# Performance work log

Measured on AMD Instinct MI355X. Metric: run time of the kernel, lower is better.

Reference implementation:

```python
import jax, jax.numpy as jnp
import numpy as np

I, H, L, O = 11, 33, 3, 18

def lstm_layer(x_tbi, W_ih, W_hh, b_ih, b_hh):
    # x_tbi: [T, B, in]; W_ih: [4H, in]; W_hh: [4H, H]
    T, B = x_tbi.shape[0], x_tbi.shape[1]
    # precompute input contribution for all timesteps (one big GEMM)
    xg = jnp.einsum('tbi,gi->tbg', x_tbi, W_ih) + b_ih + b_hh  # [T, B, 4H]
    h0 = jnp.zeros((B, H), x_tbi.dtype)
    c0 = jnp.zeros((B, H), x_tbi.dtype)

    def step(carry, xg_t):
        h, c = carry
        gates = xg_t + h @ W_hh.T                      # [B, 4H]
        i, f, g, o = jnp.split(gates, 4, axis=-1)      # PyTorch gate order i,f,g,o
        i = jax.nn.sigmoid(i)
        f = jax.nn.sigmoid(f)
        g = jnp.tanh(g)
        o = jax.nn.sigmoid(o)
        c = f * c + i * g
        h = o * jnp.tanh(c)
        return (h, c), h

    (hT, cT), ys = jax.lax.scan(step, (h0, c0), xg)
    return ys, hT, cT  # ys: [T, B, H]


def setup_inputs() -> dict:
    key = jax.random.key(0)
    ks = jax.random.split(key, 20)
    B, T = 512, 2048
    s = 1.0 / np.sqrt(H)
    d = {'x': jax.random.normal(ks[0], (B, T, I), jnp.float32)}
    in_sizes = [I, H, H]
    for l in range(L):
        d[f'W_ih{l}'] = jax.random.uniform(ks[1 + 4 * l], (4 * H, in_sizes[l]), jnp.float32, -s, s)
        d[f'W_hh{l}'] = jax.random.uniform(ks[2 + 4 * l], (4 * H, H), jnp.float32, -s, s)
        d[f'b_ih{l}'] = jax.random.uniform(ks[3 + 4 * l], (4 * H,), jnp.float32, -s, s)
        d[f'b_hh{l}'] = jax.random.uniform(ks[4 + 4 * l], (4 * H,), jnp.float32, -s, s)
    d['W1'] = jax.random.normal(ks[13], (4 * O, H), jnp.float32) * 0.05
    d['b1'] = jnp.zeros((4 * O,), jnp.float32)
    d['W2'] = jax.random.normal(ks[14], (O, 4 * O), jnp.float32) * 0.05
    d['b2'] = jnp.zeros((O,), jnp.float32)
    return d


def reference(x, W_ih0, W_hh0, b_ih0, b_hh0, W_ih1, W_hh1, b_ih1, b_hh1,
              W_ih2, W_hh2, b_ih2, b_hh2, W1, b1, W2, b2):
    # x: [B, T, I] (batch_first) -> time-major for scan
    xt = jnp.transpose(x, (1, 0, 2))  # [T, B, I]
    params = [(W_ih0, W_hh0, b_ih0, b_hh0),
              (W_ih1, W_hh1, b_ih1, b_hh1),
              (W_ih2, W_hh2, b_ih2, b_hh2)]
    hiddens = []
    cur = xt
    for (Wi, Wh, bi, bh) in params:
        cur, hT, _ = lstm_layer(cur, Wi, Wh, bi, bh)
        hiddens.append(hT)
    hidden = jnp.stack(hiddens, axis=0)  # [L, B, H] (final hidden state per layer)
    # MLP head (dropout inactive at inference); torch nn.GELU default = exact erf
    h1 = jax.nn.gelu(hidden @ W1.T + b1, approximate=False)
    out = h1 @ W2.T + b2  # [L, B, O]
    return out, hidden
```

## Files before the change

kernel.cpp:

```cpp
#include <hip/hip_runtime.h>
#include <math.h>

#define TT 2048
#define BB 512
#define II 11
#define HH 33
#define NL 3
#define OO 18
#define HSLOT 48

typedef _Float16 h2 __attribute__((ext_vector_type(2)));
typedef _Float16 h8 __attribute__((ext_vector_type(8)));

__device__ __forceinline__ float sigm_f(float x) {
    float e = __expf(-x);
    return __builtin_amdgcn_rcpf(1.0f + e);
}
__device__ __forceinline__ float tanh_f(float x) {
    float e = __expf(2.0f * x);
    return 1.0f - 2.0f * __builtin_amdgcn_rcpf(e + 1.0f);
}

__device__ __forceinline__ h8 gldh8(const float* p, int k0, int rem) {
    h8 v;
    #pragma unroll
    for (int i = 0; i < 8; ++i) v[i] = (_Float16)((k0 + i < rem) ? p[k0 + i] : 0.0f);
    return v;
}
__device__ __forceinline__ h2 gldh2(const float* p, int k0, int rem) {
    h2 v;
    v.x = (_Float16)((k0 + 0 < rem) ? p[k0 + 0] : 0.0f);
    v.y = (_Float16)((k0 + 1 < rem) ? p[k0 + 1] : 0.0f);
    return v;
}

#define D8(a, v, w) do { \
    a = __builtin_amdgcn_fdot2((v).s01, (w).s01, a, false); \
    a = __builtin_amdgcn_fdot2((v).s23, (w).s23, a, false); \
    a = __builtin_amdgcn_fdot2((v).s45, (w).s45, a, false); \
    a = __builtin_amdgcn_fdot2((v).s67, (w).s67, a, false); } while (0)
#define D1(a, v, w) a = __builtin_amdgcn_fdot2((v), (w), a, false)

__global__ __launch_bounds__(128, 1) void lstm_pipeline_kernel(
    const float* __restrict__ x,
    const float* __restrict__ Wih0, const float* __restrict__ Whh0,
    const float* __restrict__ bih0, const float* __restrict__ bhh0,
    const float* __restrict__ Wih1, const float* __restrict__ Whh1,
    const float* __restrict__ bih1, const float* __restrict__ bhh1,
    const float* __restrict__ Wih2, const float* __restrict__ Whh2,
    const float* __restrict__ bih2, const float* __restrict__ bhh2,
    const float* __restrict__ W1, const float* __restrict__ b1,
    const float* __restrict__ W2, const float* __restrict__ b2,
    float* __restrict__ hidden_out,
    float* __restrict__ outp)
{
    __shared__ __align__(16) _Float16 buf[2][NL + 1][HSLOT];
    __shared__ float hfin[NL][HH + 1];
    __shared__ float h1s[NL][4 * OO];

    const int tid = threadIdx.x;
    const int bg  = blockIdx.x;

    for (int i = tid; i < 2 * (NL + 1) * HSLOT; i += 128)
        ((_Float16*)buf)[i] = (_Float16)0.0f;

    const bool comp = (tid < 99);
    const int  u    = tid;
    const int  l    = (u < 33) ? 0 : (u < 66) ? 1 : 2;
    const int  j    = u - 33 * l;

    const int  pi   = tid - 99;
    const bool pref = (pi >= 0) && (pi < II);
    const float* xrow = x + (size_t)bg * TT * II + (pref ? pi : 0);

    h8 z8 = {0,0,0,0,0,0,0,0};
    h2 z2 = {(_Float16)0.0f, (_Float16)0.0f};
    h8 x00=z8,x01=z8,x02=z8,x03=z8; h2 x0t=z2;
    h8 x10=z8,x11=z8,x12=z8,x13=z8; h2 x1t=z2;
    h8 x20=z8,x21=z8,x22=z8,x23=z8; h2 x2t=z2;
    h8 x30=z8,x31=z8,x32=z8,x33=z8; h2 x3t=z2;
    h8 h00=z8,h01=z8,h02=z8,h03=z8; h2 h0t=z2;
    h8 h10=z8,h11=z8,h12=z8,h13=z8; h2 h1t=z2;
    h8 h20=z8,h21=z8,h22=z8,h23=z8; h2 h2t=z2;
    h8 h30=z8,h31=z8,h32=z8,h33=z8; h2 h3t=z2;
    float b0 = 0.0f, b1v = 0.0f, b2v = 0.0f, b3v = 0.0f;

    if (comp) {
        const float* bip = (l == 0) ? bih0 : (l == 1) ? bih1 : bih2;
        const float* bhp = (l == 0) ? bhh0 : (l == 1) ? bhh1 : bhh2;
        b0  = bip[0 * HH + j] + bhp[0 * HH + j];
        b1v = bip[1 * HH + j] + bhp[1 * HH + j];
        b2v = bip[2 * HH + j] + bhp[2 * HH + j];
        b3v = bip[3 * HH + j] + bhp[3 * HH + j];

        const float* Wi = (l == 0) ? Wih0 : (l == 1) ? Wih1 : Wih2;
        const float* Wh = (l == 0) ? Whh0 : (l == 1) ? Whh1 : Whh2;
        const int kin = (l == 0) ? II : HH;
        const float* r0 = Wi + (0 * HH + j) * kin;
        const float* r1 = Wi + (1 * HH + j) * kin;
        const float* r2 = Wi + (2 * HH + j) * kin;
        const float* r3 = Wi + (3 * HH + j) * kin;
        x00=gldh8(r0,0,kin); x01=gldh8(r0,8,kin); x02=gldh8(r0,16,kin); x03=gldh8(r0,24,kin); x0t=gldh2(r0,32,kin);
        x10=gldh8(r1,0,kin); x11=gldh8(r1,8,kin); x12=gldh8(r1,16,kin); x13=gldh8(r1,24,kin); x1t=gldh2(r1,32,kin);
        x20=gldh8(r2,0,kin); x21=gldh8(r2,8,kin); x22=gldh8(r2,16,kin); x23=gldh8(r2,24,kin); x2t=gldh2(r2,32,kin);
        x30=gldh8(r3,0,kin); x31=gldh8(r3,8,kin); x32=gldh8(r3,16,kin); x33=gldh8(r3,24,kin); x3t=gldh2(r3,32,kin);
        const float* s0 = Wh + (0 * HH + j) * HH;
        const float* s1 = Wh + (1 * HH + j) * HH;
        const float* s2 = Wh + (2 * HH + j) * HH;
        const float* s3 = Wh + (3 * HH + j) * HH;
        h00=gldh8(s0,0,HH); h01=gldh8(s0,8,HH); h02=gldh8(s0,16,HH); h03=gldh8(s0,24,HH); h0t=gldh2(s0,32,HH);
        h10=gldh8(s1,0,HH); h11=gldh8(s1,8,HH); h12=gldh8(s1,16,HH); h13=gldh8(s1,24,HH); h1t=gldh2(s1,32,HH);
        h20=gldh8(s2,0,HH); h21=gldh8(s2,8,HH); h22=gldh8(s2,16,HH); h23=gldh8(s2,24,HH); h2t=gldh2(s2,32,HH);
        h30=gldh8(s3,0,HH); h31=gldh8(s3,8,HH); h32=gldh8(s3,16,HH); h33=gldh8(s3,24,HH); h3t=gldh2(s3,32,HH);
    }

    __syncthreads();
    float v_next = 0.0f, v_next2 = 0.0f;
    if (pref) {
        buf[0][0][pi] = (_Float16)xrow[0];
        v_next  = xrow[II];
        v_next2 = xrow[2 * II];
    }
    __syncthreads();

    float c = 0.0f;

    const _Float16* rin[2]  = { &buf[0][l][0],     &buf[1][l][0] };
    const _Float16* rown[2] = { &buf[0][l + 1][0], &buf[1][l + 1][0] };
    _Float16*       wrp[2]  = { &buf[0][l + 1][j], &buf[1][l + 1][j] };
    _Float16*       pxp[2]  = { &buf[0][0][pi],    &buf[1][0][pi] };

    auto step = [&](int s, int rp, bool check, bool out, bool xload, bool xstore)
        __attribute__((always_inline)) {
        const int wp = rp ^ 1;
        if (pref) {
            if (xstore) *pxp[wp] = (_Float16)v_next;
            v_next = v_next2;
            if (xload) v_next2 = xrow[(size_t)(s + 3) * II];
        }
        const bool active = check ? (comp && (s >= l) && (s - l < TT)) : comp;
        if (active) {
            const h8* VI = (const h8*)rin[rp];
            const h8 vi0 = VI[0], vi1 = VI[1], vi2 = VI[2], vi3 = VI[3];
            const h2 vit = *(const h2*)(rin[rp] + 32);
            const h8* VO = (const h8*)rown[rp];
            const h8 vo0 = VO[0], vo1 = VO[1], vo2 = VO[2], vo3 = VO[3];
            const h2 vot = *(const h2*)(rown[rp] + 32);

            float a0 = b0, a1 = b1v;
            D8(a1, vi0, x10); D8(a0, vi0, x00);
            D8(a1, vi1, x11); D8(a0, vi1, x01);
            D8(a1, vi2, x12); D8(a0, vi2, x02);
            D8(a1, vi3, x13); D8(a0, vi3, x03);
            D1(a1, vit, x1t); D1(a0, vit, x0t);
            D8(a1, vo0, h10); D8(a0, vo0, h00);
            D8(a1, vo1, h11); D8(a0, vo1, h01);
            D8(a1, vo2, h12); D8(a0, vo2, h02);
            D8(a1, vo3, h13); D8(a0, vo3, h03);
            D1(a1, vot, h1t); D1(a0, vot, h0t);
            const float fg = sigm_f(a1);
            const float ig = sigm_f(a0);

            float a2 = b2v, a3 = b3v;
            D8(a2, vi0, x20); D8(a3, vi0, x30);
            D8(a2, vi1, x21); D8(a3, vi1, x31);
            D8(a2, vi2, x22); D8(a3, vi2, x32);
            D8(a2, vi3, x23); D8(a3, vi3, x33);
            D1(a2, vit, x2t); D1(a3, vit, x3t);
            D8(a2, vo0, h20); D8(a3, vo0, h30);
            D8(a2, vo1, h21); D8(a3, vo1, h31);
            D8(a2, vo2, h22); D8(a3, vo2, h32);
            D8(a2, vo3, h23); D8(a3, vo3, h33);
            D1(a2, vot, h2t); D1(a3, vot, h3t);

            const float gg = tanh_f(a2);
            const float og = sigm_f(a3);
            c = __builtin_fmaf(fg, c, ig * gg);
            const float hnew = og * tanh_f(c);

            *wrp[wp] = (_Float16)hnew;
            if (out && (s - l == TT - 1)) {
                hidden_out[((size_t)l * BB + bg) * HH + j] = hnew;
                hfin[l][j] = hnew;
            }
        }
        __syncthreads();
    };

    step(0, 0, true, false, true, true);
    step(1, 1, true, false, true, true);
    for (int s = 2; s < TT - 4; s += 2) {
        step(s,     0, false, false, true, true);
        step(s + 1, 1, false, false, true, true);
    }
    step(TT - 4, 0, false, false, true,  true);
    step(TT - 3, 1, false, false, false, true);
    step(TT - 2, 0, false, false, false, true);
    step(TT - 1, 1, false, true,  false, false);
    step(TT,     0, true,  true,  false, false);
    step(TT + 1, 1, true,  true,  false, false);

    if (tid < 4 * OO) {
        #pragma unroll
        for (int ml = 0; ml < NL; ++ml) {
            float a = b1[tid];
            #pragma unroll
            for (int k = 0; k < HH; ++k) a += hfin[ml][k] * W1[tid * HH + k];
            h1s[ml][tid] = 0.5f * a * (1.0f + erff(a * 0.70710678118654752f));
        }
    }
    __syncthreads();
    if (tid < NL * OO) {
        const int ol = tid / OO, o = tid % OO;
        float a = b2[o];
        #pragma unroll
        for (int m = 0; m < 4 * OO; ++m) a += h1s[ol][m] * W2[o * (4 * OO) + m];
        outp[((size_t)ol * BB + bg) * OO + o] = a;
    }
}

extern "C" void kernel_launch(void* const* d_in, const int* in_sizes, int n_in,
                              void* d_out, int out_size, void* d_ws, size_t ws_size,
                              hipStream_t stream) {
    const float* x    = (const float*)d_in[0];
    const float* Wih0 = (const float*)d_in[1];
    const float* Whh0 = (const float*)d_in[2];
    const float* bih0 = (const float*)d_in[3];
    const float* bhh0 = (const float*)d_in[4];
    const float* Wih1 = (const float*)d_in[5];
    const float* Whh1 = (const float*)d_in[6];
    const float* bih1 = (const float*)d_in[7];
    const float* bhh1 = (const float*)d_in[8];
    const float* Wih2 = (const float*)d_in[9];
    const float* Whh2 = (const float*)d_in[10];
    const float* bih2 = (const float*)d_in[11];
    const float* bhh2 = (const float*)d_in[12];
    const float* W1   = (const float*)d_in[13];
    const float* b1   = (const float*)d_in[14];
    const float* W2   = (const float*)d_in[15];
    const float* b2   = (const float*)d_in[16];

    float* out    = (float*)d_out;
    float* hidden = out + NL * BB * OO;

    lstm_pipeline_kernel<<<BB, 128, 0, stream>>>(
        x, Wih0, Whh0, bih0, bhh0, Wih1, Whh1, bih1, bhh1,
        Wih2, Whh2, bih2, bhh2, W1, b1, W2, b2, hidden, out);
}
```

Before: 1.053 ms.

## Split each LSTM hidden unit across two lanes with DPP reduction

Each hidden unit is now computed by a lane pair, each lane covering half of the K dimension, and the partial gate sums are combined with a DPP quad-perm swap. The transcendental work is also split: one lane evaluates the i/g pair through a parameterised sigmoid/tanh formula and the other evaluates f/o, and the results are exchanged via DPP. Block size doubles to 256 threads with launch bounds (256,2). The aim is to shorten the serial per-timestep critical path, at the cost of extra cross-lane ops, more waves hitting each barrier, and higher register pressure per block.

```diff
diff --git a/kernel.cpp b/kernel.cpp
--- a/kernel.cpp
+++ b/kernel.cpp
@@ -21,6 +21,11 @@
     return 1.0f - 2.0f * __builtin_amdgcn_rcpf(e + 1.0f);
 }
 
+__device__ __forceinline__ float dppx1(float v) {
+    return __int_as_float(__builtin_amdgcn_update_dpp(
+        0, __float_as_int(v), 0xB1 , 0xF, 0xF, true));
+}
+
 __device__ __forceinline__ h8 gldh8(const float* p, int k0, int rem) {
     h8 v;
     #pragma unroll
@@ -34,14 +39,21 @@
     return v;
 }
 
-#define D8(a, v, w) do { \
-    a = __builtin_amdgcn_fdot2((v).s01, (w).s01, a, false); \
-    a = __builtin_amdgcn_fdot2((v).s23, (w).s23, a, false); \
-    a = __builtin_amdgcn_fdot2((v).s45, (w).s45, a, false); \
-    a = __builtin_amdgcn_fdot2((v).s67, (w).s67, a, false); } while (0)
-#define D1(a, v, w) a = __builtin_amdgcn_fdot2((v), (w), a, false)
-
-__global__ __launch_bounds__(128, 1) void lstm_pipeline_kernel(
+#define FD(a, p, q) a = __builtin_amdgcn_fdot2((p), (q), a, false)
+#define DQ(v, W0, W1, W2, W3) do { \
+    FD(a0, (v).s01, (W0).s01); FD(a1, (v).s01, (W1).s01); FD(a2, (v).s01, (W2).s01); FD(a3, (v).s01, (W3).s01); \
+    FD(a0, (v).s23, (W0).s23); FD(a1, (v).s23, (W1).s23); FD(a2, (v).s23, (W2).s23); FD(a3, (v).s23, (W3).s23); \
+    FD(a0, (v).s45, (W0).s45); FD(a1, (v).s45, (W1).s45); FD(a2, (v).s45, (W2).s45); FD(a3, (v).s45, (W3).s45); \
+    FD(a0, (v).s67, (W0).s67); FD(a1, (v).s67, (W1).s67); FD(a2, (v).s67, (W2).s67); FD(a3, (v).s67, (W3).s67); \
+} while (0)
+#define D1Q(v) do { \
+    FD(a0, (v), wi0t); FD(a1, (v), wi1t); FD(a2, (v), wi2t); FD(a3, (v), wi3t); \
+} while (0)
+#define D1QH(v) do { \
+    FD(a0, (v), wh0t); FD(a1, (v), wh1t); FD(a2, (v), wh2t); FD(a3, (v), wh3t); \
+} while (0)
+
+__global__ __launch_bounds__(256, 2) void lstm_pipeline_kernel(
     const float* __restrict__ x,
     const float* __restrict__ Wih0, const float* __restrict__ Whh0,
     const float* __restrict__ bih0, const float* __restrict__ bhh0,
@@ -61,38 +73,38 @@
     const int tid = threadIdx.x;
     const int bg  = blockIdx.x;
 
-    for (int i = tid; i < 2 * (NL + 1) * HSLOT; i += 128)
+    for (int i = tid; i < 2 * (NL + 1) * HSLOT; i += 256)
         ((_Float16*)buf)[i] = (_Float16)0.0f;
 
-    const bool comp = (tid < 99);
-    const int  u    = tid;
+    const bool comp = (tid < 2 * 99);
+    const int  u    = tid >> 1;
+    const int  hf   = tid & 1;
     const int  l    = (u < 33) ? 0 : (u < 66) ? 1 : 2;
     const int  j    = u - 33 * l;
-
-    const int  pi   = tid - 99;
+    const int  koff = hf ? 16 : 0;
+
+    const int  pi   = tid - 200;
     const bool pref = (pi >= 0) && (pi < II);
-    const float* xrow = x + (size_t)bg * TT * II + (pref ? pi : 0);
+    const int  pic  = pref ? pi : 0;
+    const float* xrow = x + (size_t)bg * TT * II + pic;
 
     h8 z8 = {0,0,0,0,0,0,0,0};
     h2 z2 = {(_Float16)0.0f, (_Float16)0.0f};
-    h8 x00=z8,x01=z8,x02=z8,x03=z8; h2 x0t=z2;
-    h8 x10=z8,x11=z8,x12=z8,x13=z8; h2 x1t=z2;
-    h8 x20=z8,x21=z8,x22=z8,x23=z8; h2 x2t=z2;
-    h8 x30=z8,x31=z8,x32=z8,x33=z8; h2 x3t=z2;
-    h8 h00=z8,h01=z8,h02=z8,h03=z8; h2 h0t=z2;
-    h8 h10=z8,h11=z8,h12=z8,h13=z8; h2 h1t=z2;
-    h8 h20=z8,h21=z8,h22=z8,h23=z8; h2 h2t=z2;
-    h8 h30=z8,h31=z8,h32=z8,h33=z8; h2 h3t=z2;
+    h8 wi00=z8,wi01=z8, wi10=z8,wi11=z8, wi20=z8,wi21=z8, wi30=z8,wi31=z8;
+    h2 wi0t=z2, wi1t=z2, wi2t=z2, wi3t=z2;
+    h8 wh00=z8,wh01=z8, wh10=z8,wh11=z8, wh20=z8,wh21=z8, wh30=z8,wh31=z8;
+    h2 wh0t=z2, wh1t=z2, wh2t=z2, wh3t=z2;
     float b0 = 0.0f, b1v = 0.0f, b2v = 0.0f, b3v = 0.0f;
 
     if (comp) {
-        const float* bip = (l == 0) ? bih0 : (l == 1) ? bih1 : bih2;
-        const float* bhp = (l == 0) ? bhh0 : (l == 1) ? bhh1 : bhh2;
-        b0  = bip[0 * HH + j] + bhp[0 * HH + j];
-        b1v = bip[1 * HH + j] + bhp[1 * HH + j];
-        b2v = bip[2 * HH + j] + bhp[2 * HH + j];
-        b3v = bip[3 * HH + j] + bhp[3 * HH + j];
-
+        if (!hf) {
+            const float* bip = (l == 0) ? bih0 : (l == 1) ? bih1 : bih2;
+            const float* bhp = (l == 0) ? bhh0 : (l == 1) ? bhh1 : bhh2;
+            b0  = bip[0 * HH + j] + bhp[0 * HH + j];
+            b1v = bip[1 * HH + j] + bhp[1 * HH + j];
+            b2v = bip[2 * HH + j] + bhp[2 * HH + j];
+            b3v = bip[3 * HH + j] + bhp[3 * HH + j];
+        }
         const float* Wi = (l == 0) ? Wih0 : (l == 1) ? Wih1 : Wih2;
         const float* Wh = (l == 0) ? Whh0 : (l == 1) ? Whh1 : Whh2;
         const int kin = (l == 0) ? II : HH;
@@ -100,19 +112,31 @@
         const float* r1 = Wi + (1 * HH + j) * kin;
         const float* r2 = Wi + (2 * HH + j) * kin;
         const float* r3 = Wi + (3 * HH + j) * kin;
-        x00=gldh8(r0,0,kin); x01=gldh8(r0,8,kin); x02=gldh8(r0,16,kin); x03=gldh8(r0,24,kin); x0t=gldh2(r0,32,kin);
-        x10=gldh8(r1,0,kin); x11=gldh8(r1,8,kin); x12=gldh8(r1,16,kin); x13=gldh8(r1,24,kin); x1t=gldh2(r1,32,kin);
-        x20=gldh8(r2,0,kin); x21=gldh8(r2,8,kin); x22=gldh8(r2,16,kin); x23=gldh8(r2,24,kin); x2t=gldh2(r2,32,kin);
-        x30=gldh8(r3,0,kin); x31=gldh8(r3,8,kin); x32=gldh8(r3,16,kin); x33=gldh8(r3,24,kin); x3t=gldh2(r3,32,kin);
-        const float* s0 = Wh + (0 * HH + j) * HH;
-        const float* s1 = Wh + (1 * HH + j) * HH;
-        const float* s2 = Wh + (2 * HH + j) * HH;
-        const float* s3 = Wh + (3 * HH + j) * HH;
-        h00=gldh8(s0,0,HH); h01=gldh8(s0,8,HH); h02=gldh8(s0,16,HH); h03=gldh8(s0,24,HH); h0t=gldh2(s0,32,HH);
-        h10=gldh8(s1,0,HH); h11=gldh8(s1,8,HH); h12=gldh8(s1,16,HH); h13=gldh8(s1,24,HH); h1t=gldh2(s1,32,HH);
-        h20=gldh8(s2,0,HH); h21=gldh8(s2,8,HH); h22=gldh8(s2,16,HH); h23=gldh8(s2,24,HH); h2t=gldh2(s2,32,HH);
-        h30=gldh8(s3,0,HH); h31=gldh8(s3,8,HH); h32=gldh8(s3,16,HH); h33=gldh8(s3,24,HH); h3t=gldh2(s3,32,HH);
-    }
+        wi00 = gldh8(r0, koff, kin); wi01 = gldh8(r0, koff + 8, kin);
+        wi10 = gldh8(r1, koff, kin); wi11 = gldh8(r1, koff + 8, kin);
+        wi20 = gldh8(r2, koff, kin); wi21 = gldh8(r2, koff + 8, kin);
+        wi30 = gldh8(r3, koff, kin); wi31 = gldh8(r3, koff + 8, kin);
+        if (hf) {
+            wi0t = gldh2(r0, 32, kin); wi1t = gldh2(r1, 32, kin);
+            wi2t = gldh2(r2, 32, kin); wi3t = gldh2(r3, 32, kin);
+        }
+        const float* s0p = Wh + (0 * HH + j) * HH;
+        const float* s1p = Wh + (1 * HH + j) * HH;
+        const float* s2p = Wh + (2 * HH + j) * HH;
+        const float* s3p = Wh + (3 * HH + j) * HH;
+        wh00 = gldh8(s0p, koff, HH); wh01 = gldh8(s0p, koff + 8, HH);
+        wh10 = gldh8(s1p, koff, HH); wh11 = gldh8(s1p, koff + 8, HH);
+        wh20 = gldh8(s2p, koff, HH); wh21 = gldh8(s2p, koff + 8, HH);
+        wh30 = gldh8(s3p, koff, HH); wh31 = gldh8(s3p, koff + 8, HH);
+        if (hf) {
+            wh0t = gldh2(s0p, 32, HH); wh1t = gldh2(s1p, 32, HH);
+            wh2t = gldh2(s2p, 32, HH); wh3t = gldh2(s3p, 32, HH);
+        }
+    }
+
+    const float kX = hf ? 2.0f : -1.0f;
+    const float AX = hf ? 1.0f : 0.0f;
+    const float BX = hf ? -2.0f : 1.0f;
 
     __syncthreads();
     float v_next = 0.0f, v_next2 = 0.0f;
@@ -128,7 +152,7 @@
     const _Float16* rin[2]  = { &buf[0][l][0],     &buf[1][l][0] };
     const _Float16* rown[2] = { &buf[0][l + 1][0], &buf[1][l + 1][0] };
     _Float16*       wrp[2]  = { &buf[0][l + 1][j], &buf[1][l + 1][j] };
-    _Float16*       pxp[2]  = { &buf[0][0][pi],    &buf[1][0][pi] };
+    _Float16*       pxp[2]  = { &buf[0][0][pic],   &buf[1][0][pic] };
 
     auto step = [&](int s, int rp, bool check, bool out, bool xload, bool xstore)
         __attribute__((always_inline)) {
@@ -140,48 +164,48 @@
         }
         const bool active = check ? (comp && (s >= l) && (s - l < TT)) : comp;
         if (active) {
-            const h8* VI = (const h8*)rin[rp];
-            const h8 vi0 = VI[0], vi1 = VI[1], vi2 = VI[2], vi3 = VI[3];
-            const h2 vit = *(const h2*)(rin[rp] + 32);
-            const h8* VO = (const h8*)rown[rp];
-            const h8 vo0 = VO[0], vo1 = VO[1], vo2 = VO[2], vo3 = VO[3];
-            const h2 vot = *(const h2*)(rown[rp] + 32);
-
-            float a0 = b0, a1 = b1v;
-            D8(a1, vi0, x10); D8(a0, vi0, x00);
-            D8(a1, vi1, x11); D8(a0, vi1, x01);
-            D8(a1, vi2, x12); D8(a0, vi2, x02);
-            D8(a1, vi3, x13); D8(a0, vi3, x03);
-            D1(a1, vit, x1t); D1(a0, vit, x0t);
-            D8(a1, vo0, h10); D8(a0, vo0, h00);
-            D8(a1, vo1, h11); D8(a0, vo1, h01);
-            D8(a1, vo2, h12); D8(a0, vo2, h02);
-            D8(a1, vo3, h13); D8(a0, vo3, h03);
-            D1(a1, vot, h1t); D1(a0, vot, h0t);
-            const float fg = sigm_f(a1);
-            const float ig = sigm_f(a0);
-
-            float a2 = b2v, a3 = b3v;
-            D8(a2, vi0, x20); D8(a3, vi0, x30);
-            D8(a2, vi1, x21); D8(a3, vi1, x31);
-            D8(a2, vi2, x22); D8(a3, vi2, x32);
-            D8(a2, vi3, x23); D8(a3, vi3, x33);
-            D1(a2, vit, x2t); D1(a3, vit, x3t);
-            D8(a2, vo0, h20); D8(a3, vo0, h30);
-            D8(a2, vo1, h21); D8(a3, vo1, h31);
-            D8(a2, vo2, h22); D8(a3, vo2, h32);
-            D8(a2, vo3, h23); D8(a3, vo3, h33);
-            D1(a2, vot, h2t); D1(a3, vot, h3t);
-
-            const float gg = tanh_f(a2);
-            const float og = sigm_f(a3);
+            const _Float16* ri = rin[rp];
+            const _Float16* ro = rown[rp];
+            const h8 vi0 = *(const h8*)(ri + koff);
+            const h8 vi1 = *(const h8*)(ri + koff + 8);
+            const h2 vit = *(const h2*)(ri + 32);
+            const h8 vo0 = *(const h8*)(ro + koff);
+            const h8 vo1 = *(const h8*)(ro + koff + 8);
+            const h2 vot = *(const h2*)(ro + 32);
+
+            float a0 = b0, a1 = b1v, a2 = b2v, a3 = b3v;
+            DQ(vi0, wi00, wi10, wi20, wi30);
+            DQ(vi1, wi01, wi11, wi21, wi31);
+            DQ(vo0, wh00, wh10, wh20, wh30);
+            DQ(vo1, wh01, wh11, wh21, wh31);
+            D1Q(vit);
+            D1QH(vot);
+
+            a0 += dppx1(a0); a1 += dppx1(a1);
+            a2 += dppx1(a2); a3 += dppx1(a3);
+
+            const float aXv = hf ? a2 : a0;
+            const float eX  = __expf(kX * aXv);
+            const float rX  = __builtin_amdgcn_rcpf(1.0f + eX);
+            const float xg  = __builtin_fmaf(BX, rX, AX);
+            const float yg  = sigm_f(hf ? a3 : a1);
+
+            const float xp = dppx1(xg);
+            const float yp = dppx1(yg);
+            const float ig = hf ? xp : xg;
+            const float fg = hf ? yp : yg;
+            const float gg = hf ? xg : xp;
+            const float og = hf ? yg : yp;
+
             c = __builtin_fmaf(fg, c, ig * gg);
             const float hnew = og * tanh_f(c);
 
-            *wrp[wp] = (_Float16)hnew;
-            if (out && (s - l == TT - 1)) {
-                hidden_out[((size_t)l * BB + bg) * HH + j] = hnew;
-                hfin[l][j] = hnew;
+            if (!hf) {
+                *wrp[wp] = (_Float16)hnew;
+                if (out && (s - l == TT - 1)) {
+                    hidden_out[((size_t)l * BB + bg) * HH + j] = hnew;
+                    hfin[l][j] = hnew;
+                }
             }
         }
         __syncthreads();
@@ -243,7 +267,7 @@
     float* out    = (float*)d_out;
     float* hidden = out + NL * BB * OO;
 
-    lstm_pipeline_kernel<<<BB, 128, 0, stream>>>(
+    lstm_pipeline_kernel<<<BB, 256, 0, stream>>>(
         x, Wih0, Whh0, bih0, bhh0, Wih1, Whh1, bih1, bhh1,
         Wih2, Whh2, bih2, bhh2, W1, b1, W2, b2, hidden, out);
 }
```

Measured after the change: 1.094 ms. 3.8% more time.

## Assign one wavefront per LSTM layer and sync per epoch of eight steps

Applied to the files above, without the earlier changes.

Each of the three layers now runs in its own 64-lane wavefront. Within a wave the recurrent state passes through LDS without block barriers for eight timesteps at a time. Layers hand outputs to the next layer through double-buffered epoch buffers, so __syncthreads runs once per eight steps instead of once per timestep. Input x is prefetched as float4 chunks per epoch. The cost is more lanes sitting idle (33 of 64 compute), a longer pipeline fill and drain, and a dependence on intra-wave LDS ordering being correct without explicit barriers.

```diff
diff --git a/kernel.cpp b/kernel.cpp
--- a/kernel.cpp
+++ b/kernel.cpp
@@ -7,7 +7,10 @@
 #define HH 33
 #define NL 3
 #define OO 18
-#define HSLOT 48
+#define SS 8
+#define EPT (TT / SS)
+#define NEP (EPT + NL - 1)
+#define HROW 40
 
 typedef _Float16 h2 __attribute__((ext_vector_type(2)));
 typedef _Float16 h8 __attribute__((ext_vector_type(8)));
@@ -34,14 +37,15 @@
     return v;
 }
 
-#define D8(a, v, w) do { \
-    a = __builtin_amdgcn_fdot2((v).s01, (w).s01, a, false); \
-    a = __builtin_amdgcn_fdot2((v).s23, (w).s23, a, false); \
-    a = __builtin_amdgcn_fdot2((v).s45, (w).s45, a, false); \
-    a = __builtin_amdgcn_fdot2((v).s67, (w).s67, a, false); } while (0)
-#define D1(a, v, w) a = __builtin_amdgcn_fdot2((v), (w), a, false)
-
-__global__ __launch_bounds__(128, 1) void lstm_pipeline_kernel(
+#define FD(a, p, q) a = __builtin_amdgcn_fdot2((p), (q), a, false)
+#define DQ4(v, w0, w1, w2, w3) do { \
+    FD(a0,(v).s01,(w0).s01); FD(a1,(v).s01,(w1).s01); FD(a2,(v).s01,(w2).s01); FD(a3,(v).s01,(w3).s01); \
+    FD(a0,(v).s23,(w0).s23); FD(a1,(v).s23,(w1).s23); FD(a2,(v).s23,(w2).s23); FD(a3,(v).s23,(w3).s23); \
+    FD(a0,(v).s45,(w0).s45); FD(a1,(v).s45,(w1).s45); FD(a2,(v).s45,(w2).s45); FD(a3,(v).s45,(w3).s45); \
+    FD(a0,(v).s67,(w0).s67); FD(a1,(v).s67,(w1).s67); FD(a2,(v).s67,(w2).s67); FD(a3,(v).s67,(w3).s67); \
+} while (0)
+
+__global__ __launch_bounds__(192, 1) void lstm_epoch_kernel(
     const float* __restrict__ x,
     const float* __restrict__ Wih0, const float* __restrict__ Whh0,
     const float* __restrict__ bih0, const float* __restrict__ bhh0,
@@ -54,24 +58,22 @@
     float* __restrict__ hidden_out,
     float* __restrict__ outp)
 {
-    __shared__ __align__(16) _Float16 buf[2][NL + 1][HSLOT];
+    __shared__ __align__(16) _Float16 xbuf[2][SS][HROW];
+    __shared__ __align__(16) _Float16 ibuf[2][2][SS][HROW];
+    __shared__ __align__(16) _Float16 hown[NL][HROW];
     __shared__ float hfin[NL][HH + 1];
     __shared__ float h1s[NL][4 * OO];
 
-    const int tid = threadIdx.x;
-    const int bg  = blockIdx.x;
-
-    for (int i = tid; i < 2 * (NL + 1) * HSLOT; i += 128)
-        ((_Float16*)buf)[i] = (_Float16)0.0f;
-
-    const bool comp = (tid < 99);
-    const int  u    = tid;
-    const int  l    = (u < 33) ? 0 : (u < 66) ? 1 : 2;
-    const int  j    = u - 33 * l;
-
-    const int  pi   = tid - 99;
-    const bool pref = (pi >= 0) && (pi < II);
-    const float* xrow = x + (size_t)bg * TT * II + (pref ? pi : 0);
+    const int tid  = threadIdx.x;
+    const int bg   = blockIdx.x;
+    const int lane = tid & 63;
+    const int wid  = tid >> 6;
+    const int j    = lane;
+    const bool cl  = (lane < HH);
+
+    for (int f = tid; f < 2 * SS * HROW; f += 192) ((_Float16*)xbuf)[f] = (_Float16)0.0f;
+    for (int f = tid; f < 2 * 2 * SS * HROW; f += 192) ((_Float16*)ibuf)[f] = (_Float16)0.0f;
+    for (int f = tid; f < NL * HROW; f += 192) ((_Float16*)hown)[f] = (_Float16)0.0f;
 
     h8 z8 = {0,0,0,0,0,0,0,0};
     h2 z2 = {(_Float16)0.0f, (_Float16)0.0f};
@@ -85,7 +87,8 @@
     h8 h30=z8,h31=z8,h32=z8,h33=z8; h2 h3t=z2;
     float b0 = 0.0f, b1v = 0.0f, b2v = 0.0f, b3v = 0.0f;
 
-    if (comp) {
+    if (cl) {
+        const int l = wid;
         const float* bip = (l == 0) ? bih0 : (l == 1) ? bih1 : bih2;
         const float* bhp = (l == 0) ? bhh0 : (l == 1) ? bhh1 : bhh2;
         b0  = bip[0 * HH + j] + bhp[0 * HH + j];
@@ -114,91 +117,111 @@
         h30=gldh8(s3,0,HH); h31=gldh8(s3,8,HH); h32=gldh8(s3,16,HH); h33=gldh8(s3,24,HH); h3t=gldh2(s3,32,HH);
     }
 
+    const int  pl   = lane - HH;
+    const bool pfl  = (wid == 0) && (pl >= 0) && (pl < 22);
+    const float* xblk = x + (size_t)bg * TT * II;
+
+    if (pfl) {
+        const float4 v = *(const float4*)(xblk + 4 * pl);
+        #pragma unroll
+        for (int q = 0; q < 4; ++q) {
+            const int f = 4 * pl + q;
+            const int t = (f * 373) >> 12;
+            const int i = f - 11 * t;
+            xbuf[0][t][i] = (_Float16)((&v.x)[q]);
+        }
+    }
     __syncthreads();
-    float v_next = 0.0f, v_next2 = 0.0f;
-    if (pref) {
-        buf[0][0][pi] = (_Float16)xrow[0];
-        v_next  = xrow[II];
-        v_next2 = xrow[2 * II];
-    }
-    __syncthreads();
 
     float c = 0.0f;
-
-    const _Float16* rin[2]  = { &buf[0][l][0],     &buf[1][l][0] };
-    const _Float16* rown[2] = { &buf[0][l + 1][0], &buf[1][l + 1][0] };
-    _Float16*       wrp[2]  = { &buf[0][l + 1][j], &buf[1][l + 1][j] };
-    _Float16*       pxp[2]  = { &buf[0][0][pi],    &buf[1][0][pi] };
-
-    auto step = [&](int s, int rp, bool check, bool out, bool xload, bool xstore)
-        __attribute__((always_inline)) {
-        const int wp = rp ^ 1;
-        if (pref) {
-            if (xstore) *pxp[wp] = (_Float16)v_next;
-            v_next = v_next2;
-            if (xload) v_next2 = xrow[(size_t)(s + 3) * II];
-        }
-        const bool active = check ? (comp && (s >= l) && (s - l < TT)) : comp;
-        if (active) {
-            const h8* VI = (const h8*)rin[rp];
-            const h8 vi0 = VI[0], vi1 = VI[1], vi2 = VI[2], vi3 = VI[3];
-            const h2 vit = *(const h2*)(rin[rp] + 32);
-            const h8* VO = (const h8*)rown[rp];
-            const h8 vo0 = VO[0], vo1 = VO[1], vo2 = VO[2], vo3 = VO[3];
-            const h2 vot = *(const h2*)(rown[rp] + 32);
-
-            float a0 = b0, a1 = b1v;
-            D8(a1, vi0, x10); D8(a0, vi0, x00);
-            D8(a1, vi1, x11); D8(a0, vi1, x01);
-            D8(a1, vi2, x12); D8(a0, vi2, x02);
-            D8(a1, vi3, x13); D8(a0, vi3, x03);
-            D1(a1, vit, x1t); D1(a0, vit, x0t);
-            D8(a1, vo0, h10); D8(a0, vo0, h00);
-            D8(a1, vo1, h11); D8(a0, vo1, h01);
-            D8(a1, vo2, h12); D8(a0, vo2, h02);
-            D8(a1, vo3, h13); D8(a0, vo3, h03);
-            D1(a1, vot, h1t); D1(a0, vot, h0t);
-            const float fg = sigm_f(a1);
-            const float ig = sigm_f(a0);
-
-            float a2 = b2v, a3 = b3v;
-            D8(a2, vi0, x20); D8(a3, vi0, x30);
-            D8(a2, vi1, x21); D8(a3, vi1, x31);
-            D8(a2, vi2, x22); D8(a3, vi2, x32);
-            D8(a2, vi3, x23); D8(a3, vi3, x33);
-            D1(a2, vit, x2t); D1(a3, vit, x3t);
-            D8(a2, vo0, h20); D8(a3, vo0, h30);
-            D8(a2, vo1, h21); D8(a3, vo1, h31);
-            D8(a2, vo2, h22); D8(a3, vo2, h32);
-            D8(a2, vo3, h23); D8(a3, vo3, h33);
-            D1(a2, vot, h2t); D1(a3, vot, h3t);
-
-            const float gg = tanh_f(a2);
-            const float og = sigm_f(a3);
-            c = __builtin_fmaf(fg, c, ig * gg);
-            const float hnew = og * tanh_f(c);
-
-            *wrp[wp] = (_Float16)hnew;
-            if (out && (s - l == TT - 1)) {
-                hidden_out[((size_t)l * BB + bg) * HH + j] = hnew;
-                hfin[l][j] = hnew;
+    const _Float16* inbase[2];
+    if (wid == 0) { inbase[0] = &xbuf[0][0][0];         inbase[1] = &xbuf[1][0][0]; }
+    else          { inbase[0] = &ibuf[0][wid - 1][0][0]; inbase[1] = &ibuf[1][wid - 1][0][0]; }
+    const int oe = (wid < 2) ? wid : 0;
+    _Float16* outb[2] = { &ibuf[1][oe][0][0], &ibuf[0][oe][0][0] };
+    _Float16* hop = &hown[wid][0];
+    const bool haveout = (wid < 2);
+
+    h8 vi0, vi1, vi2, vi3; h2 vit;
+    h8 vo0, vo1, vo2, vo3; h2 vot;
+
+    for (int e = 0; e < NEP; ++e) {
+        const int par = e & 1;
+
+        float4 pv;
+        const bool pf = pfl && (e < EPT - 1);
+        if (pf) pv = *(const float4*)(xblk + (size_t)(e + 1) * (SS * II) + 4 * pl);
+
+        const bool act = (e >= wid) && (e - wid < EPT);
+        if (act) {
+            const _Float16* inb  = inbase[par];
+            _Float16*       ob   = outb[par];
+            const bool      last = (e == EPT - 1 + wid);
+
+            vi0 = ((const h8*)inb)[0]; vi1 = ((const h8*)inb)[1];
+            vi2 = ((const h8*)inb)[2]; vi3 = ((const h8*)inb)[3];
+            vit = *(const h2*)(inb + 32);
+            vo0 = ((const h8*)hop)[0]; vo1 = ((const h8*)hop)[1];
+            vo2 = ((const h8*)hop)[2]; vo3 = ((const h8*)hop)[3];
+            vot = *(const h2*)(hop + 32);
+
+            auto step = [&](int k) __attribute__((always_inline)) {
+                float a0 = b0, a1 = b1v, a2 = b2v, a3 = b3v;
+                DQ4(vi0, x00, x10, x20, x30);
+                DQ4(vi1, x01, x11, x21, x31);
+                DQ4(vi2, x02, x12, x22, x32);
+                DQ4(vi3, x03, x13, x23, x33);
+                FD(a0, vit, x0t); FD(a1, vit, x1t);
+                FD(a2, vit, x2t); FD(a3, vit, x3t);
+                DQ4(vo0, h00, h10, h20, h30);
+                DQ4(vo1, h01, h11, h21, h31);
+                DQ4(vo2, h02, h12, h22, h32);
+                DQ4(vo3, h03, h13, h23, h33);
+                FD(a0, vot, h0t); FD(a1, vot, h1t);
+                FD(a2, vot, h2t); FD(a3, vot, h3t);
+                if (k < SS - 1) {
+                    const _Float16* r = inb + (k + 1) * HROW;
+                    vi0 = ((const h8*)r)[0]; vi1 = ((const h8*)r)[1];
+                    vi2 = ((const h8*)r)[2]; vi3 = ((const h8*)r)[3];
+                    vit = *(const h2*)(r + 32);
+                }
+                const float ig = sigm_f(a0);
+                const float fg = sigm_f(a1);
+                const float gg = tanh_f(a2);
+                const float og = sigm_f(a3);
+                c = __builtin_fmaf(fg, c, ig * gg);
+                const float hnew = og * tanh_f(c);
+                const _Float16 h16 = (_Float16)hnew;
+                if (cl) {
+                    hop[j] = h16;
+                    if (haveout) ob[k * HROW + j] = h16;
+                }
+                if (k == SS - 1 && last && cl) {
+                    hidden_out[((size_t)wid * BB + bg) * HH + j] = hnew;
+                    hfin[wid][j] = hnew;
+                }
+                if (k < SS - 1) {
+                    vo0 = ((const h8*)hop)[0]; vo1 = ((const h8*)hop)[1];
+                    vo2 = ((const h8*)hop)[2]; vo3 = ((const h8*)hop)[3];
+                    vot = *(const h2*)(hop + 32);
+                }
+            };
+            step(0); step(1); step(2); step(3);
+            step(4); step(5); step(6); step(7);
+        }
+
+        if (pf) {
+            _Float16* xw = &xbuf[par ^ 1][0][0];
+            #pragma unroll
+            for (int q = 0; q < 4; ++q) {
+                const int f = 4 * pl + q;
+                const int t = (f * 373) >> 12;
+                const int i = f - 11 * t;
+                xw[t * HROW + i] = (_Float16)((&pv.x)[q]);
             }
         }
         __syncthreads();
-    };
-
-    step(0, 0, true, false, true, true);
-    step(1, 1, true, false, true, true);
-    for (int s = 2; s < TT - 4; s += 2) {
-        step(s,     0, false, false, true, true);
-        step(s + 1, 1, false, false, true, true);
-    }
-    step(TT - 4, 0, false, false, true,  true);
-    step(TT - 3, 1, false, false, false, true);
-    step(TT - 2, 0, false, false, false, true);
-    step(TT - 1, 1, false, true,  false, false);
-    step(TT,     0, true,  true,  false, false);
-    step(TT + 1, 1, true,  true,  false, false);
+    }
 
     if (tid < 4 * OO) {
         #pragma unroll
@@ -243,7 +266,7 @@
     float* out    = (float*)d_out;
     float* hidden = out + NL * BB * OO;
 
-    lstm_pipeline_kernel<<<BB, 128, 0, stream>>>(
+    lstm_epoch_kernel<<<BB, 192, 0, stream>>>(
         x, Wih0, Whh0, bih0, bhh0, Wih1, Whh1, bih1, bhh1,
         Wih2, Whh2, bih2, bhh2, W1, b1, W2, b2, hidden, out);
 }
```

Result: slower. 1.859 ms (+76.4%).
